# Optimization experiments

Hardware: AMD Instinct MI355X
Metric: run time of the kernel (lower is better)

The kernel has to match this reference:

```python
import jax, jax.numpy as jnp
import numpy as np

B, S, D, H = 4, 2048, 1024, 16
DK = D // H

def setup_inputs() -> dict:
    key = jax.random.key(0)
    ks = jax.random.split(key, 5)
    scale = 1.0 / np.sqrt(D)
    return {
        "x": jax.random.normal(ks[0], (B, S, D), dtype=jnp.float32),
        "Wq": jax.random.normal(ks[1], (H, D, DK), dtype=jnp.float32) * scale,
        "Wk": jax.random.normal(ks[2], (H, D, DK), dtype=jnp.float32) * scale,
        "Wv": jax.random.normal(ks[3], (H, D, DK), dtype=jnp.float32) * scale,
        "Wo": jax.random.normal(ks[4], (D, D), dtype=jnp.float32) * scale,
    }

def reference(x, Wq, Wk, Wv, Wo):
    # x: [B,S,D]; Wq/Wk/Wv: [H,D,DK] (stacked per-head Linear weights); Wo: [D,D]
    seq = x.shape[-2]
    q = jnp.einsum('bsd,hdk->bhsk', x, Wq)
    k = jnp.einsum('bsd,hdk->bhsk', x, Wk)
    v = jnp.einsum('bsd,hdk->bhsk', x, Wv)
    dk = q.shape[-1]
    scores = jnp.einsum('bhqk,bhsk->bhqs', q, k) / jnp.sqrt(jnp.asarray(dk, x.dtype))
    # causal mask: mask out strictly-future positions (triu, diagonal=1)
    causal = jnp.tril(jnp.ones((seq, seq), dtype=bool))  # True = keep
    scores = jnp.where(causal, scores, -jnp.inf)
    probs = jax.nn.softmax(scores, axis=-1)  # attn_pdrop = 0.0 -> dropout is identity
    attn = jnp.einsum('bhqs,bhsk->bhqk', probs, v)
    # concat heads: [B,S,H*DK]
    concat = attn.transpose(0, 2, 1, 3).reshape(x.shape[0], seq, -1)
    # output_proj: nn.Linear(D, D, bias=False) -> y = concat @ Wo.T
    return jnp.einsum('bsd,ed->bse', concat, Wo)
```

## Files before the change

kernel.cpp:

```cpp
#include <hip/hip_runtime.h>
#include <hip/hip_bf16.h>

#define B_ 4
#define S_ 2048
#define D_ 1024
#define H_ 16
#define DK_ 64

typedef __attribute__((ext_vector_type(8))) short bf16x8;
typedef __attribute__((ext_vector_type(4))) float f32x4;
typedef __attribute__((ext_vector_type(4))) unsigned int u32x4;

__device__ __forceinline__ unsigned short f2bf(float f) {
    unsigned int u = __float_as_uint(f);
    u += 0x7FFFu + ((u >> 16) & 1u);
    return (unsigned short)(u >> 16);
}

__global__ void cvt_kernel(const float* __restrict__ src, unsigned short* __restrict__ dst) {
    int i = (blockIdx.x * 256 + threadIdx.x) * 8;
    float4 f0 = *(const float4*)&src[i];
    float4 f1 = *(const float4*)&src[i + 4];
    unsigned short t[8] __attribute__((aligned(16))) = {
        f2bf(f0.x), f2bf(f0.y), f2bf(f0.z), f2bf(f0.w),
        f2bf(f1.x), f2bf(f1.y), f2bf(f1.z), f2bf(f1.w)};
    *(u32x4*)&dst[i] = *(const u32x4*)t;
}

__global__ void prepack_kernel(const float* __restrict__ Wq,
                               const float* __restrict__ Wk,
                               const float* __restrict__ Wv,
                               unsigned short* __restrict__ Wt) {
    __shared__ unsigned short Ts[64 * 65];
    int h = blockIdx.x, w3 = blockIdx.y, t = blockIdx.z;
    const float* src = (w3 == 0 ? Wq : (w3 == 1 ? Wk : Wv)) + h * D_ * DK_ + t * 64 * DK_;
    unsigned short* dst = Wt + (w3 * H_ + h) * DK_ * D_ + t * 64;
    int tid = threadIdx.x;
    for (int rep = 0; rep < 16; ++rep) {
        int idx = rep * 256 + tid;
        int dl = idx >> 6, k = idx & 63;
        Ts[k * 65 + dl] = f2bf(src[dl * 64 + k]);
    }
    __syncthreads();
    for (int rep = 0; rep < 16; ++rep) {
        int idx = rep * 256 + tid;
        int kl = idx >> 6, dl = idx & 63;
        dst[kl * D_ + dl] = Ts[kl * 65 + dl];
    }
}

__device__ __forceinline__ void stage128_async(const unsigned short* __restrict__ g,
                                               unsigned short* lds_base, int wv, int lane, int ldg) {
#pragma unroll
    for (int it = 0; it < 4; ++it) {
        int rbase = wv * 32 + it * 8;
        int r = rbase + (lane >> 3);
        int gc = (lane & 7) ^ ((lane >> 3) & 7);
        const unsigned short* gp = g + r * ldg + gc * 8;
        unsigned short* lp = lds_base + rbase * 64;
        __builtin_amdgcn_global_load_lds((const __attribute__((address_space(1))) unsigned int*)gp,
                                         (__attribute__((address_space(3))) unsigned int*)lp,
                                         16, 0, 0);
    }
}

__device__ __forceinline__ void stage64_async(const unsigned short* __restrict__ g,
                                              unsigned short* lds_base, int wv, int lane, int ldg) {
#pragma unroll
    for (int it = 0; it < 2; ++it) {
        int rbase = wv * 16 + it * 8;
        int r = rbase + (lane >> 3);
        int gc = (lane & 7) ^ ((lane >> 3) & 7);
        const unsigned short* gp = g + r * ldg + gc * 8;
        unsigned short* lp = lds_base + rbase * 64;
        __builtin_amdgcn_global_load_lds((const __attribute__((address_space(1))) unsigned int*)gp,
                                         (__attribute__((address_space(3))) unsigned int*)lp,
                                         16, 0, 0);
    }
}

template <bool QKV_OUT>
__global__ __launch_bounds__(256) void gemm128_kernel(const unsigned short* __restrict__ A,
                                                      const unsigned short* __restrict__ Bt,
                                                      void* __restrict__ Out,
                                                      unsigned short* __restrict__ VtOut) {
    __shared__ __align__(16) unsigned short smem[2 * 128 * 64];
    unsigned short* As = smem;
    unsigned short* Bs = smem + 128 * 64;
    const int tid = threadIdx.x;
    const int wv = tid >> 6, lane = tid & 63, l15 = lane & 15, q4 = lane >> 4;
    const int wm = wv >> 1, wn = wv & 1;
    const int r0 = blockIdx.x * 128, c0 = blockIdx.y * 128;

    const unsigned short* Ab = A + r0 * D_;
    const unsigned short* Bb = Bt + c0 * D_;

    f32x4 acc[4][4] = {};

    for (int kt = 0; kt < 16; ++kt) {
        stage128_async(Ab + kt * 64, As, wv, lane, D_);
        stage128_async(Bb + kt * 64, Bs, wv, lane, D_);
        __syncthreads();
#pragma unroll
        for (int kk = 0; kk < 2; ++kk) {
            bf16x8 af[4], bf[4];
            const int sw = ((kk * 4 + q4) ^ (l15 & 7)) * 8;
#pragma unroll
            for (int i = 0; i < 4; ++i) {
                af[i] = *(const bf16x8*)&As[(wm * 64 + i * 16 + l15) * 64 + sw];
                bf[i] = *(const bf16x8*)&Bs[(wn * 64 + i * 16 + l15) * 64 + sw];
            }
#pragma unroll
            for (int i = 0; i < 4; ++i)
#pragma unroll
                for (int j = 0; j < 4; ++j)
                    acc[i][j] = __builtin_amdgcn_mfma_f32_16x16x32_bf16(af[i], bf[j], acc[i][j], 0, 0, 0);
        }
        __syncthreads();
    }

    if (QKV_OUT && c0 >= 2 * D_) {
        const int b = r0 >> 11, s0 = r0 & (S_ - 1);
#pragma unroll
        for (int i = 0; i < 4; ++i)
#pragma unroll
            for (int j = 0; j < 4; ++j)
#pragma unroll
                for (int rr = 0; rr < 4; ++rr) {
                    int col = wn * 64 + j * 16 + l15;
                    int row = wm * 64 + i * 16 + q4 * 4 + rr;
                    smem[col * 128 + (row ^ ((col & 7) * 8))] = f2bf(acc[i][j][rr]);
                }
        __syncthreads();
#pragma unroll
        for (int rep = 0; rep < 8; ++rep) {
            int idx = rep * 256 + tid;
            int col = idx >> 4, ch = idx & 15;
            u32x4 v = *(const u32x4*)&smem[col * 128 + ((ch * 8) ^ ((col & 7) * 8))];
            int gcol = c0 + col;
            int vrow = b * 1024 + (gcol & 1023);
            *(u32x4*)&VtOut[vrow * S_ + s0 + ch * 8] = v;
        }
    } else {
#pragma unroll
        for (int i = 0; i < 4; ++i)
#pragma unroll
            for (int j = 0; j < 4; ++j)
#pragma unroll
                for (int rr = 0; rr < 4; ++rr) {
                    int grow = r0 + wm * 64 + i * 16 + q4 * 4 + rr;
                    int gcol = c0 + wn * 64 + j * 16 + l15;
                    if (QKV_OUT) {
                        int b = grow >> 11, s = grow & (S_ - 1);
                        int w3 = gcol >> 10, h = (gcol >> 6) & 15, dk = gcol & 63;
                        ((unsigned short*)Out)[(((w3 * B_ + b) * H_ + h) * S_ + s) * DK_ + dk] =
                            f2bf(acc[i][j][rr]);
                    } else {
                        ((float*)Out)[grow * D_ + gcol] = acc[i][j][rr];
                    }
                }
    }
}

__global__ __launch_bounds__(256) void attn_kernel(const unsigned short* __restrict__ qkv,
                                                   unsigned short* __restrict__ concat) {
    const int bh = blockIdx.x;
    const int pr = blockIdx.y;
    const int b = bh >> 4, h = bh & 15;
    const unsigned short* Qp = qkv + ((0 * B_ + b) * H_ + h) * S_ * DK_;
    const unsigned short* Kp = qkv + ((1 * B_ + b) * H_ + h) * S_ * DK_;
    const unsigned short* Vt = qkv + 2 * B_ * H_ * S_ * DK_ + (b * H_ + h) * DK_ * S_;

    __shared__ __align__(16) unsigned short Kb[2][64 * 64];
    __shared__ __align__(16) unsigned short Vb[2][64 * 64];
    __shared__ __align__(16) unsigned short Ps[4][32 * 64];

    const int tid = threadIdx.x;
    const int wv = tid >> 6, lane = tid & 63, l15 = lane & 15, q4 = lane >> 4;

    const float cs = 0.125f * 1.44269504088896340736f;
    const float MB = 16.0f;

    for (int side = 0; side < 2; ++side) {
        const int q0 = (side == 0 ? pr : 15 - pr) * 128;
        const int nk = q0 / 64 + 2;

        stage64_async(Kp + 0 * DK_, Kb[0], wv, lane, DK_);
        stage64_async(Vt + 0, Vb[0], wv, lane, S_);

        bf16x8 aq[2][2];
#pragma unroll
        for (int rt = 0; rt < 2; ++rt)
#pragma unroll
            for (int kk = 0; kk < 2; ++kk)
                aq[rt][kk] = *(const bf16x8*)&Qp[(q0 + wv * 32 + rt * 16 + l15) * DK_ + kk * 32 + q4 * 8];

        f32x4 o[2][4] = {};
        float l_[2][4] = {};

        __syncthreads();

        for (int t = 0; t < nk; ++t) {
            const int k0 = t * 64;
            if (t + 1 < nk) {
                stage64_async(Kp + (k0 + 64) * DK_, Kb[(t + 1) & 1], wv, lane, DK_);
                stage64_async(Vt + (k0 + 64), Vb[(t + 1) & 1], wv, lane, S_);
            }
            const unsigned short* Kt = Kb[t & 1];
            const unsigned short* Vtt = Vb[t & 1];

            f32x4 sa[2][4] = {};
#pragma unroll
            for (int kk = 0; kk < 2; ++kk) {
                const int sw = ((kk * 4 + q4) ^ (l15 & 7)) * 8;
#pragma unroll
                for (int ct = 0; ct < 4; ++ct) {
                    bf16x8 bk = *(const bf16x8*)&Kt[(ct * 16 + l15) * 64 + sw];
                    sa[0][ct] = __builtin_amdgcn_mfma_f32_16x16x32_bf16(aq[0][kk], bk, sa[0][ct], 0, 0, 0);
                    sa[1][ct] = __builtin_amdgcn_mfma_f32_16x16x32_bf16(aq[1][kk], bk, sa[1][ct], 0, 0, 0);
                }
            }

            if (t < nk - 2) {
#pragma unroll
                for (int rt = 0; rt < 2; ++rt)
#pragma unroll
                    for (int ct = 0; ct < 4; ++ct)
#pragma unroll
                        for (int r = 0; r < 4; ++r) {
                            float p = exp2f(sa[rt][ct][r] * cs - MB);
                            l_[rt][r] += p;
                            int q = wv * 32 + rt * 16 + q4 * 4 + r;
                            int ql = rt * 16 + q4 * 4 + r;
                            (void)q;
                            Ps[wv][ql * 64 + ((ct * 16 + l15) ^ ((ql & 7) * 8))] = f2bf(p);
                        }
            } else {
#pragma unroll
                for (int rt = 0; rt < 2; ++rt) {
                    const int qrow_base = q0 + wv * 32 + rt * 16 + q4 * 4;
#pragma unroll
                    for (int ct = 0; ct < 4; ++ct) {
                        int col = k0 + ct * 16 + l15;
#pragma unroll
                        for (int r = 0; r < 4; ++r) {
                            float a = (col <= qrow_base + r) ? sa[rt][ct][r] * cs - MB : -1000.0f;
                            float p = exp2f(a);
                            l_[rt][r] += p;
                            int ql = rt * 16 + q4 * 4 + r;
                            Ps[wv][ql * 64 + ((ct * 16 + l15) ^ ((ql & 7) * 8))] = f2bf(p);
                        }
                    }
                }
            }

#pragma unroll
            for (int kk = 0; kk < 2; ++kk) {
                bf16x8 ap0 = *(const bf16x8*)&Ps[wv][(l15) * 64 + ((kk * 32 + q4 * 8) ^ ((l15 & 7) * 8))];
                bf16x8 ap1 = *(const bf16x8*)&Ps[wv][(16 + l15) * 64 + ((kk * 32 + q4 * 8) ^ ((l15 & 7) * 8))];
                const int sw = ((kk * 4 + q4) ^ (l15 & 7)) * 8;
#pragma unroll
                for (int cd = 0; cd < 4; ++cd) {
                    bf16x8 bv = *(const bf16x8*)&Vtt[(cd * 16 + l15) * 64 + sw];
                    o[0][cd] = __builtin_amdgcn_mfma_f32_16x16x32_bf16(ap0, bv, o[0][cd], 0, 0, 0);
                    o[1][cd] = __builtin_amdgcn_mfma_f32_16x16x32_bf16(ap1, bv, o[1][cd], 0, 0, 0);
                }
            }
            __syncthreads();
        }

#pragma unroll
        for (int rt = 0; rt < 2; ++rt)
#pragma unroll
            for (int r = 0; r < 4; ++r) {
                float lr = l_[rt][r];
                lr += __shfl_xor(lr, 1);
                lr += __shfl_xor(lr, 2);
                lr += __shfl_xor(lr, 4);
                lr += __shfl_xor(lr, 8);
                float inv = 1.0f / fmaxf(lr, 1.0e-37f);
                int row = q0 + wv * 32 + rt * 16 + q4 * 4 + r;
#pragma unroll
                for (int cd = 0; cd < 4; ++cd) {
                    int col = h * DK_ + cd * 16 + l15;
                    concat[(b * S_ + row) * D_ + col] = f2bf(o[rt][cd][r] * inv);
                }
            }
        __syncthreads();
    }
}

extern "C" void kernel_launch(void* const* d_in, const int* in_sizes, int n_in,
                              void* d_out, int out_size, void* d_ws, size_t ws_size,
                              hipStream_t stream) {
    const float* x  = (const float*)d_in[0];
    const float* Wq = (const float*)d_in[1];
    const float* Wk = (const float*)d_in[2];
    const float* Wv = (const float*)d_in[3];
    const float* Wo = (const float*)d_in[4];

    unsigned short* qkv    = (unsigned short*)d_ws;
    unsigned short* Wt     = qkv + 3 * B_ * H_ * S_ * DK_;
    unsigned short* xbf    = Wt + 3 * H_ * DK_ * D_;
    unsigned short* concat = xbf;
    unsigned short* Wobf   = Wt;
    unsigned short* VtOut  = qkv + 2 * B_ * H_ * S_ * DK_;

    cvt_kernel<<<B_ * S_ * D_ / 2048, 256, 0, stream>>>(x, xbf);
    prepack_kernel<<<dim3(H_, 3, 16), 256, 0, stream>>>(Wq, Wk, Wv, Wt);
    gemm128_kernel<true><<<dim3(B_ * S_ / 128, 3 * H_ * DK_ / 128), 256, 0, stream>>>(xbf, Wt, qkv, VtOut);
    cvt_kernel<<<D_ * D_ / 2048, 256, 0, stream>>>(Wo, Wobf);
    attn_kernel<<<dim3(64, 8), 256, 0, stream>>>(qkv, concat);
    gemm128_kernel<false><<<dim3(B_ * S_ / 128, D_ / 128), 256, 0, stream>>>(concat, Wobf, d_out, nullptr);
}
```

Baseline: 265.0 us.

## Keep attention probabilities in registers and fold softmax scale into Wq

```diff
diff --git a/kernel.cpp b/kernel.cpp
--- a/kernel.cpp
+++ b/kernel.cpp
@@ -15,6 +15,12 @@
     unsigned int u = __float_as_uint(f);
     u += 0x7FFFu + ((u >> 16) & 1u);
     return (unsigned short)(u >> 16);
+}
+
+__device__ __forceinline__ unsigned int cvtpk_bf16(float lo, float hi) {
+    unsigned int r;
+    asm("v_cvt_pk_bf16_f32 %0, %1, %2" : "=v"(r) : "v"(lo), "v"(hi));
+    return r;
 }
 
 __global__ void cvt_kernel(const float* __restrict__ src, unsigned short* __restrict__ dst) {
@@ -35,11 +41,12 @@
     int h = blockIdx.x, w3 = blockIdx.y, t = blockIdx.z;
     const float* src = (w3 == 0 ? Wq : (w3 == 1 ? Wk : Wv)) + h * D_ * DK_ + t * 64 * DK_;
     unsigned short* dst = Wt + (w3 * H_ + h) * DK_ * D_ + t * 64;
+    const float wscale = (w3 == 0) ? 0.18033688011112042f : 1.0f;
     int tid = threadIdx.x;
     for (int rep = 0; rep < 16; ++rep) {
         int idx = rep * 256 + tid;
         int dl = idx >> 6, k = idx & 63;
-        Ts[k * 65 + dl] = f2bf(src[dl * 64 + k]);
+        Ts[k * 65 + dl] = f2bf(src[dl * 64 + k] * wscale);
     }
     __syncthreads();
     for (int rep = 0; rep < 16; ++rep) {
@@ -173,20 +180,16 @@
 
     __shared__ __align__(16) unsigned short Kb[2][64 * 64];
     __shared__ __align__(16) unsigned short Vb[2][64 * 64];
-    __shared__ __align__(16) unsigned short Ps[4][32 * 64];
 
     const int tid = threadIdx.x;
     const int wv = tid >> 6, lane = tid & 63, l15 = lane & 15, q4 = lane >> 4;
-
-    const float cs = 0.125f * 1.44269504088896340736f;
-    const float MB = 16.0f;
 
     for (int side = 0; side < 2; ++side) {
         const int q0 = (side == 0 ? pr : 15 - pr) * 128;
         const int nk = q0 / 64 + 2;
 
-        stage64_async(Kp + 0 * DK_, Kb[0], wv, lane, DK_);
-        stage64_async(Vt + 0, Vb[0], wv, lane, S_);
+        stage64_async(Kp, Kb[0], wv, lane, DK_);
+        stage64_async(Vt, Vb[0], wv, lane, S_);
 
         bf16x8 aq[2][2];
 #pragma unroll
@@ -196,7 +199,7 @@
                 aq[rt][kk] = *(const bf16x8*)&Qp[(q0 + wv * 32 + rt * 16 + l15) * DK_ + kk * 32 + q4 * 8];
 
         f32x4 o[2][4] = {};
-        float l_[2][4] = {};
+        float l_[2] = {0.0f, 0.0f};
 
         __syncthreads();
 
@@ -209,76 +212,93 @@
             const unsigned short* Kt = Kb[t & 1];
             const unsigned short* Vtt = Vb[t & 1];
 
-            f32x4 sa[2][4] = {};
-#pragma unroll
-            for (int kk = 0; kk < 2; ++kk) {
-                const int sw = ((kk * 4 + q4) ^ (l15 & 7)) * 8;
-#pragma unroll
-                for (int ct = 0; ct < 4; ++ct) {
-                    bf16x8 bk = *(const bf16x8*)&Kt[(ct * 16 + l15) * 64 + sw];
-                    sa[0][ct] = __builtin_amdgcn_mfma_f32_16x16x32_bf16(aq[0][kk], bk, sa[0][ct], 0, 0, 0);
-                    sa[1][ct] = __builtin_amdgcn_mfma_f32_16x16x32_bf16(aq[1][kk], bk, sa[1][ct], 0, 0, 0);
-                }
-            }
-
-            if (t < nk - 2) {
+            if ((t + 1 < nk) || (wv >= 2)) {
+                f32x4 sa[2][4] = {};
+                __builtin_amdgcn_s_setprio(1);
+#pragma unroll
+                for (int kk = 0; kk < 2; ++kk) {
+                    const int sw = ((kk * 4 + q4) ^ (l15 & 7)) * 8;
+#pragma unroll
+                    for (int ct = 0; ct < 4; ++ct) {
+                        bf16x8 bk = *(const bf16x8*)&Kt[(ct * 16 + l15) * 64 + sw];
+                        sa[0][ct] = __builtin_amdgcn_mfma_f32_16x16x32_bf16(bk, aq[0][kk], sa[0][ct], 0, 0, 0);
+                        sa[1][ct] = __builtin_amdgcn_mfma_f32_16x16x32_bf16(bk, aq[1][kk], sa[1][ct], 0, 0, 0);
+                    }
+                }
+                __builtin_amdgcn_s_setprio(0);
+
+                if (t < nk - 2) {
+#pragma unroll
+                    for (int rt = 0; rt < 2; ++rt)
+#pragma unroll
+                        for (int ct = 0; ct < 4; ++ct)
+#pragma unroll
+                            for (int r = 0; r < 4; ++r)
+                                sa[rt][ct][r] = __builtin_amdgcn_exp2f(sa[rt][ct][r]);
+                } else {
+                    const int kb = k0 + q4 * 4;
+#pragma unroll
+                    for (int rt = 0; rt < 2; ++rt) {
+                        const int qrow = q0 + wv * 32 + rt * 16 + l15;
+#pragma unroll
+                        for (int ct = 0; ct < 4; ++ct)
+#pragma unroll
+                            for (int r = 0; r < 4; ++r) {
+                                float e = __builtin_amdgcn_exp2f(sa[rt][ct][r]);
+                                sa[rt][ct][r] = (kb + ct * 16 + r <= qrow) ? e : 0.0f;
+                            }
+                    }
+                }
+
 #pragma unroll
                 for (int rt = 0; rt < 2; ++rt)
 #pragma unroll
                     for (int ct = 0; ct < 4; ++ct)
-#pragma unroll
-                        for (int r = 0; r < 4; ++r) {
-                            float p = exp2f(sa[rt][ct][r] * cs - MB);
-                            l_[rt][r] += p;
-                            int q = wv * 32 + rt * 16 + q4 * 4 + r;
-                            int ql = rt * 16 + q4 * 4 + r;
-                            (void)q;
-                            Ps[wv][ql * 64 + ((ct * 16 + l15) ^ ((ql & 7) * 8))] = f2bf(p);
+                        l_[rt] += (sa[rt][ct][0] + sa[rt][ct][1]) + (sa[rt][ct][2] + sa[rt][ct][3]);
+
+                bf16x8 F[2][2];
+#pragma unroll
+                for (int rt = 0; rt < 2; ++rt)
+#pragma unroll
+                    for (int kk = 0; kk < 2; ++kk) {
+                        u32x4 w;
+#pragma unroll
+                        for (int u = 0; u < 2; ++u) {
+                            unsigned int a = cvtpk_bf16(sa[rt][2 * kk][2 * u], sa[rt][2 * kk][2 * u + 1]);
+                            unsigned int c = cvtpk_bf16(sa[rt][2 * kk + 1][2 * u], sa[rt][2 * kk + 1][2 * u + 1]);
+                            asm("v_permlane32_swap_b32 %0, %1" : "+v"(a), "+v"(c));
+                            asm("v_permlane16_swap_b32 %0, %1" : "+v"(a), "+v"(c));
+                            w[u] = a;
+                            w[2 + u] = c;
                         }
-            } else {
-#pragma unroll
-                for (int rt = 0; rt < 2; ++rt) {
-                    const int qrow_base = q0 + wv * 32 + rt * 16 + q4 * 4;
-#pragma unroll
-                    for (int ct = 0; ct < 4; ++ct) {
-                        int col = k0 + ct * 16 + l15;
-#pragma unroll
-                        for (int r = 0; r < 4; ++r) {
-                            float a = (col <= qrow_base + r) ? sa[rt][ct][r] * cs - MB : -1000.0f;
-                            float p = exp2f(a);
-                            l_[rt][r] += p;
-                            int ql = rt * 16 + q4 * 4 + r;
-                            Ps[wv][ql * 64 + ((ct * 16 + l15) ^ ((ql & 7) * 8))] = f2bf(p);
-                        }
-                    }
-                }
-            }
-
-#pragma unroll
-            for (int kk = 0; kk < 2; ++kk) {
-                bf16x8 ap0 = *(const bf16x8*)&Ps[wv][(l15) * 64 + ((kk * 32 + q4 * 8) ^ ((l15 & 7) * 8))];
-                bf16x8 ap1 = *(const bf16x8*)&Ps[wv][(16 + l15) * 64 + ((kk * 32 + q4 * 8) ^ ((l15 & 7) * 8))];
-                const int sw = ((kk * 4 + q4) ^ (l15 & 7)) * 8;
-#pragma unroll
-                for (int cd = 0; cd < 4; ++cd) {
-                    bf16x8 bv = *(const bf16x8*)&Vtt[(cd * 16 + l15) * 64 + sw];
-                    o[0][cd] = __builtin_amdgcn_mfma_f32_16x16x32_bf16(ap0, bv, o[0][cd], 0, 0, 0);
-                    o[1][cd] = __builtin_amdgcn_mfma_f32_16x16x32_bf16(ap1, bv, o[1][cd], 0, 0, 0);
-                }
+                        F[rt][kk] = *(const bf16x8*)&w;
+                    }
+
+                __builtin_amdgcn_s_setprio(1);
+#pragma unroll
+                for (int kk = 0; kk < 2; ++kk) {
+                    const int sw = ((kk * 4 + q4) ^ (l15 & 7)) * 8;
+#pragma unroll
+                    for (int cd = 0; cd < 4; ++cd) {
+                        bf16x8 bv = *(const bf16x8*)&Vtt[(cd * 16 + l15) * 64 + sw];
+                        o[0][cd] = __builtin_amdgcn_mfma_f32_16x16x32_bf16(F[0][kk], bv, o[0][cd], 0, 0, 0);
+                        o[1][cd] = __builtin_amdgcn_mfma_f32_16x16x32_bf16(F[1][kk], bv, o[1][cd], 0, 0, 0);
+                    }
+                }
+                __builtin_amdgcn_s_setprio(0);
             }
             __syncthreads();
         }
 
 #pragma unroll
-        for (int rt = 0; rt < 2; ++rt)
+        for (int rt = 0; rt < 2; ++rt) {
+            float lr = l_[rt];
+            lr += __shfl_xor(lr, 16);
+            lr += __shfl_xor(lr, 32);
 #pragma unroll
             for (int r = 0; r < 4; ++r) {
-                float lr = l_[rt][r];
-                lr += __shfl_xor(lr, 1);
-                lr += __shfl_xor(lr, 2);
-                lr += __shfl_xor(lr, 4);
-                lr += __shfl_xor(lr, 8);
-                float inv = 1.0f / fmaxf(lr, 1.0e-37f);
+                float lfull = __shfl(lr, (lane & 48) | (q4 * 4 + r));
+                float inv = 1.0f / fmaxf(lfull, 1.0e-37f);
                 int row = q0 + wv * 32 + rt * 16 + q4 * 4 + r;
 #pragma unroll
                 for (int cd = 0; cd < 4; ++cd) {
@@ -286,6 +306,7 @@
                     concat[(b * S_ + row) * D_ + col] = f2bf(o[rt][cd][r] * inv);
                 }
             }
+        }
         __syncthreads();
     }
 }
```

Measured after the change: 248.6 us. 1.07x faster.
